# Kernel optimization log

Measured on AMD Instinct MI355X. Metric: run time of the kernel, lower is better.

The kernel has to match this reference:

```python
import jax, jax.numpy as jnp
from jax import lax
import numpy as np

B, T, D, H, W = 1, 32, 32, 64, 64
NE, EXPAND = 4, 2          # num_experts, ffn expand
F = 2 * D                   # real-ified channel count
FH = EXPAND * F
NOISE_SCALE = 0.01
LN_EPS = 1e-5


def _pscan(A, X):
    # first-order linear recurrence y_t = A_t*y_{t-1} + X_t, scan over axis=1
    def comb(l, r):
        a1, x1 = l
        a2, x2 = r
        return (a1 * a2, a2 * x1 + x2)
    return lax.associative_scan(comb, (A, X), axis=1)[1]


def _ln(v, g, b):
    # v: (N, C, H, W); LayerNorm over channel dim (matches permute->LN->permute)
    v = jnp.moveaxis(v, 1, -1)
    m = v.mean(-1, keepdims=True)
    s = v.var(-1, keepdims=True)
    v = (v - m) * lax.rsqrt(s + LN_EPS) * g + b
    return jnp.moveaxis(v, -1, 1)


def setup_inputs() -> dict:
    key = jax.random.key(0)
    ks = jax.random.split(key, 24)
    def rn(i, shape, s=1.0):
        return jax.random.normal(ks[i], shape, jnp.float32) * s
    return {
        "x_re": rn(0, (B, T, D, H, W)),
        "x_im": rn(1, (B, T, D, H, W)),
        "dt": jax.random.uniform(ks[2], (T,), jnp.float32, 0.5, 1.5),
        "eps_re": rn(3, (B, T, H, W, D)),
        "eps_im": rn(4, (B, T, H, W, D)),
        "ln1_g": jnp.ones((F,), jnp.float32), "ln1_b": jnp.zeros((F,), jnp.float32),
        "ln2_g": jnp.ones((F,), jnp.float32), "ln2_b": jnp.zeros((F,), jnp.float32),
        "conv_w": rn(5, (F, F, 3, 3), 0.05), "conv_b": rn(6, (F,), 0.01),
        "enc_re": rn(7, (D, D), D ** -0.5), "enc_im": rn(8, (D, D), D ** -0.5),
        "dec_re": rn(9, (D, D), D ** -0.5), "dec_im": rn(10, (D, D), D ** -0.5),
        "lam_re": rn(11, (D,), 0.5), "lam_im": rn(12, (D,)),
        "flux_alpha": rn(13, (D,)),
        "flux_wre": rn(14, (D, D), 0.1), "flux_wim": rn(15, (D, D), 0.1),
        "wg": rn(16, (F, NE), 0.1),
        "w1": rn(17, (NE, F, FH), 0.05), "b1": jnp.zeros((NE, FH), jnp.float32),
        "w2": rn(18, (NE, FH, F), 0.05), "b2": jnp.zeros((NE, F), jnp.float32),
    }


def reference(x_re, x_im, dt, eps_re, eps_im, ln1_g, ln1_b, ln2_g, ln2_b,
              conv_w, conv_b, enc_re, enc_im, dec_re, dec_im, lam_re, lam_im,
              flux_alpha, flux_wre, flux_wim, wg, w1, b1, w2, b2):
    x = x_re + 1j * x_im                                   # (B,T,D,H,W) complex
    b_, t_, d_, h_, w_ = x.shape
    # --- spatial branch: LN over 2D real channels + Clifford-style conv ---
    xr = jnp.concatenate([x_re, x_im], axis=2).reshape(b_ * t_, 2 * d_, h_, w_)
    xn = _ln(xr, ln1_g, ln1_b)
    xs = lax.conv_general_dilated(xn, conv_w, (1, 1), 'SAME',
                                  dimension_numbers=('NCHW', 'OIHW', 'NCHW'))
    xs = xs + conv_b[None, :, None, None]
    xs_c = xs[:, :d_] + 1j * xs[:, d_:]
    xs5 = xs_c.reshape(b_, t_, d_, h_, w_)
    # --- eigenbasis encode (channels-last complex matmul) ---
    xcl = jnp.transpose(xs5, (0, 1, 3, 4, 2))              # (B,T,H,W,D)
    u = xcl @ (enc_re + 1j * enc_im)
    # --- global flux tracker pscan over T ---
    x_mean = xs5.mean(axis=(-2, -1))                       # (B,T,D) complex
    flux_A = jnp.broadcast_to(jax.nn.sigmoid(flux_alpha).astype(x.dtype), x_mean.shape)
    flux_X = x_mean @ (flux_wre + 1j * flux_wim)
    flux_seq = _pscan(flux_A, flux_X)                      # (B,T,D)
    # --- temporal transition operators per step ---
    lam = -jax.nn.softplus(lam_re) + 1j * lam_im           # (D,) stable decay
    dtc = dt.astype(jnp.float32)[:, None]                  # (T,1)
    op_decay = jnp.exp(lam[None, :] * dtc)                 # (T,D) complex
    op_forcing = (op_decay - 1.0) / lam[None, :]
    u_scaled = u * op_forcing[None, :, None, None, :]
    A_time = jnp.broadcast_to(op_decay[None, :, None, None, :], u.shape)
    Y = _pscan(A_time, u_scaled)                           # (B,T,H,W,D)
    # --- state-dependent stochastic term ---
    eps = eps_re + 1j * eps_im
    noise = NOISE_SCALE * jnp.sqrt(dt)[None, :, None, None, None] * Y * eps
    u_out = Y + noise
    # --- decode + temporal LN ---
    x_out = u_out @ (dec_re + 1j * dec_im)                 # (B,T,H,W,D)
    x_out = jnp.transpose(x_out, (0, 1, 4, 2, 3)).reshape(b_ * t_, d_, h_, w_)
    xo_r = jnp.concatenate([x_out.real, x_out.imag], axis=1)
    xo_n = _ln(xo_r, ln2_g, ln2_b)
    xoc = xo_n[:, :d_] + 1j * xo_n[:, d_:]
    # --- gated dense-MoE FFN on real-ified channels-last features ---
    f = jnp.moveaxis(xo_n, 1, -1)                          # (BT,H,W,2D)
    gate = jax.nn.softmax(f @ wg, axis=-1)                 # (BT,H,W,E)
    hdn = jax.nn.gelu(jnp.einsum('nhwc,ecf->nhwef', f, w1) + b1)
    eo = jnp.einsum('nhwef,efc->nhwec', hdn, w2) + b2
    delta_f = jnp.einsum('nhwec,nhwe->nhwc', eo, gate)
    delta = delta_f[..., :d_] + 1j * delta_f[..., d_:]
    delta = jnp.moveaxis(delta, -1, 1)                     # (BT,D,H,W)
    out = x + (xoc + delta).reshape(b_, t_, d_, h_, w_)
    flux_last = flux_seq[:, -1]
    return (jnp.stack([out.real, out.imag], axis=0),
            jnp.stack([flux_last.real, flux_last.imag], axis=0))
```

## Files before the change

### kernel.cpp

```cpp
#include <hip/hip_runtime.h>
#include <math.h>

#define PX 4096
#define TT 32
#define DD 32
#define CC 64
#define PW 66
#define PPX 4356

typedef __attribute__((ext_vector_type(8))) short short8v;
typedef __attribute__((ext_vector_type(4))) float f32x4;

__device__ __forceinline__ float gelu_fast(float x) {
    float u = x * x;
    float a = x * (1.5957691216057308f + 0.07135481627f * u);
    return x / (1.0f + __expf(-a));
}

__device__ __forceinline__ unsigned short f2b(float x) {
    union { float f; unsigned u; } v; v.f = x;
    unsigned r = v.u + 0x7FFF + ((v.u >> 16) & 1);
    return (unsigned short)(r >> 16);
}

__device__ __forceinline__ float b2f(unsigned short b) {
    union { unsigned u; float f; } v; v.u = ((unsigned)b) << 16;
    return v.f;
}

__global__ __launch_bounds__(256) void k1_ln1(
        const float* __restrict__ xre, const float* __restrict__ xim,
        const float* __restrict__ g, const float* __restrict__ b,
        unsigned short* __restrict__ xpad) {
    int gid = blockIdx.x * 256 + threadIdx.x;
    int t = gid >> 12, px = gid & 4095;
    int row = px >> 6, col = px & 63;
    const float* pr = xre + (size_t)t * DD * PX + px;
    const float* pi = xim + (size_t)t * DD * PX + px;
    float s = 0.f, ss = 0.f;
    #pragma unroll
    for (int d = 0; d < DD; ++d) {
        float vr = pr[d * PX], vi = pi[d * PX];
        s += vr + vi; ss += vr * vr + vi * vi;
    }
    float m = s * (1.f / 64.f);
    float var = ss * (1.f / 64.f) - m * m;
    float rs = rsqrtf(var + 1e-5f);
    unsigned short* o = xpad + ((size_t)t * PPX + (row + 1) * PW + (col + 1)) * 64;
    #pragma unroll
    for (int j = 0; j < 8; ++j) {
        short8v v8;
        #pragma unroll
        for (int dd = 0; dd < 8; ++dd) {
            int ch = j * 8 + dd;
            float v = (ch < 32) ? (pr[ch * PX] - m) * rs * g[ch] + b[ch]
                                : (pi[(ch - 32) * PX] - m) * rs * g[ch] + b[ch];
            v8[dd] = (short)f2b(v);
        }
        *(short8v*)&o[j * 8] = v8;
    }
}

__global__ __launch_bounds__(256) void k0_prep(
        const float* __restrict__ w1, const float* __restrict__ w2,
        const float* __restrict__ convw,
        const float* __restrict__ encre, const float* __restrict__ encim,
        const float* __restrict__ decre, const float* __restrict__ decim,
        unsigned short* __restrict__ w1t, unsigned short* __restrict__ w2t,
        unsigned short* __restrict__ w9t,
        unsigned short* __restrict__ benct, unsigned short* __restrict__ bdect,
        unsigned short* __restrict__ xpad) {
    int gid = blockIdx.x * 256 + threadIdx.x;
    if (gid < 32768) {
        int idx = gid;
        int e = idx >> 13, r = idx & 8191;
        int f = r >> 6, p = r & 63;
        int c = (p & 7) + 8 * ((p >> 3) ^ (f & 7));
        w1t[idx] = f2b(w1[((size_t)e * 64 + c) * 128 + f]);
    } else if (gid < 65536) {
        int idx = gid - 32768;
        int e = idx >> 13, r = idx & 8191;
        int n = r >> 7, p = r & 127;
        int f = (p & 7) + 8 * ((p >> 3) ^ (n & 7));
        w2t[idx] = f2b(w2[((size_t)e * 128 + f) * 64 + n]);
    } else if (gid < 102400) {
        int idx = gid - 65536;
        int tap = idx >> 12, rem = idx & 4095;
        int n = rem >> 6, p = rem & 63;
        int k = (p & 7) + 8 * ((p >> 3) ^ (n & 7));
        w9t[idx] = f2b(convw[((size_t)n * 64 + k) * 9 + tap]);
    } else if (gid < 110592) {
        int idx = gid - 102400;
        const float* Rr = (idx < 4096) ? encre : decre;
        const float* Ri = (idx < 4096) ? encim : decim;
        unsigned short* dst = (idx < 4096) ? benct : bdect;
        idx &= 4095;
        int n = idx >> 6, p = idx & 63;
        int k = (p & 7) + 8 * ((p >> 3) ^ (n & 7));
        float v;
        if (n < 32) v = (k < 32) ? Rr[k * 32 + n] : -Ri[(k - 32) * 32 + n];
        else        v = (k < 32) ? Ri[k * 32 + (n - 32)] : Rr[(k - 32) * 32 + (n - 32)];
        dst[idx] = f2b(v);
    } else if (gid < 110592 + 32 * 260) {
        int idx = gid - 110592;
        int im = idx / 260, h = idx % 260;
        int row, col;
        if (h < 66)       { row = 0;  col = h; }
        else if (h < 132) { row = 65; col = h - 66; }
        else { int hh = h - 132; row = 1 + (hh >> 1); col = (hh & 1) * 65; }
        unsigned short* p = xpad + ((size_t)im * PPX + row * PW + col) * 64;
        short8v z = (short8v)0;
        #pragma unroll
        for (int j = 0; j < 8; ++j) *(short8v*)&p[j * 8] = z;
    }
}

__global__ __launch_bounds__(256, 2) void k2_conv(
        const unsigned short* __restrict__ xpad,
        const unsigned short* __restrict__ w9t,
        const float* __restrict__ bias, float* __restrict__ xs) {
    __shared__ __align__(16) unsigned short wst[36864];
    int tid = threadIdx.x;
    int bid = blockIdx.x;
    int lb = (bid & 7) * 64 + (bid >> 3);
    int t = lb >> 4, rg = lb & 15;
    int lane = tid & 63, wv = tid >> 6;
    int l15 = lane & 15, g = lane >> 4;
    #pragma unroll
    for (int i = 0; i < 18; ++i) {
        int idx = i * 256 + tid;
        *(short8v*)&wst[idx * 8] = *(const short8v*)&w9t[idx * 8];
    }
    __syncthreads();
    int r = rg * 4 + wv;
    const unsigned short* xb = xpad + (size_t)t * PPX * 64;
    f32x4 acc[4][4];
    #pragma unroll
    for (int m = 0; m < 4; ++m)
        #pragma unroll
        for (int nt = 0; nt < 4; ++nt) acc[m][nt] = (f32x4)0.f;

    #pragma unroll
    for (int kh = 0; kh < 3; ++kh) {
        #pragma unroll
        for (int kw = 0; kw < 3; ++kw) {
            int tap = kh * 3 + kw;
            #pragma unroll
            for (int kc = 0; kc < 2; ++kc) {
                short8v a[4];
                #pragma unroll
                for (int m = 0; m < 4; ++m) {
                    int pcol = m * 16 + l15 + kw;
                    a[m] = *(const short8v*)&xb[((size_t)(r + kh) * PW + pcol) * 64 + kc * 32 + g * 8];
                }
                #pragma unroll
                for (int nt = 0; nt < 4; ++nt) {
                    int n = nt * 16 + l15;
                    short8v bf = *(const short8v*)&wst[tap * 4096 + n * 64 + ((kc * 4 + g) ^ (n & 7)) * 8];
                    #pragma unroll
                    for (int m = 0; m < 4; ++m)
                        acc[m][nt] = __builtin_amdgcn_mfma_f32_16x16x32_bf16(a[m], bf, acc[m][nt], 0, 0, 0);
                }
            }
        }
    }
    float* dst = xs + ((size_t)t * PX + r * 64) * 64;
    #pragma unroll
    for (int nt = 0; nt < 4; ++nt) {
        float bo = bias[nt * 16 + l15];
        #pragma unroll
        for (int m = 0; m < 4; ++m) {
            #pragma unroll
            for (int reg = 0; reg < 4; ++reg) {
                int tok = m * 16 + g * 4 + reg;
                dst[(size_t)tok * 64 + nt * 16 + l15] = acc[m][nt][reg] + bo;
            }
        }
    }
}

__global__ __launch_bounds__(256) void k3_mean(
        const float* __restrict__ xs, float* __restrict__ mpart) {
    __shared__ f32x4 red[256];
    int t = blockIdx.x >> 4, sl = blockIdx.x & 15;
    int c4 = threadIdx.x & 15, q = threadIdx.x >> 4;
    const float* base = xs + ((size_t)t * PX + sl * 256) * 64 + c4 * 4;
    f32x4 s = (f32x4)0.f;
    for (int px = q; px < 256; px += 16)
        s += *(const f32x4*)&base[(size_t)px * 64];
    red[threadIdx.x] = s;
    __syncthreads();
    for (int st = 8; st > 0; st >>= 1) {
        if (q < st) red[q * 16 + c4] += red[(q + st) * 16 + c4];
        __syncthreads();
    }
    if (q == 0)
        *(f32x4*)&mpart[((size_t)t * 16 + sl) * 64 + c4 * 4] = red[c4];
}

__global__ __launch_bounds__(256) void k4_ops(
        const float* __restrict__ dt, const float* __restrict__ lam_re,
        const float* __restrict__ lam_im, const float* __restrict__ alpha,
        const float* __restrict__ wre, const float* __restrict__ wim,
        const float* __restrict__ mpart, float* __restrict__ tabs,
        float* __restrict__ outflux) {
    __shared__ float meanl[2048];
    int tid = threadIdx.x;
    for (int idx = tid; idx < 2048; idx += 256) {
        int t = idx >> 6, c = idx & 63;
        float s = 0.f;
        #pragma unroll
        for (int p = 0; p < 16; ++p) s += mpart[((size_t)t * 16 + p) * 64 + c];
        meanl[idx] = s * (1.f / 4096.f);
    }
    __syncthreads();
    for (int idx = tid; idx < 1024; idx += 256) {
        int t = idx >> 5, d = idx & 31;
        float x = lam_re[d];
        float sp = (x > 0.f) ? x + log1pf(expf(-x)) : log1pf(expf(x));
        float lr = -sp, li = lam_im[d];
        float dtv = dt[t];
        float er = expf(lr * dtv);
        float dr = er * cosf(li * dtv);
        float di = er * sinf(li * dtv);
        float den = lr * lr + li * li;
        float fr = ((dr - 1.f) * lr + di * li) / den;
        float fi = (di * lr - (dr - 1.f) * li) / den;
        tabs[idx] = dr; tabs[1024 + idx] = di;
        tabs[2048 + idx] = fr; tabs[3072 + idx] = fi;
    }
    if (tid < 32) {
        int d = tid;
        float a = 1.f / (1.f + expf(-alpha[d]));
        float yr = 0.f, yi = 0.f;
        for (int t = 0; t < 32; ++t) {
            float xr = 0.f, xi = 0.f;
            for (int k = 0; k < 32; ++k) {
                float mr = meanl[t * 64 + k], mi = meanl[t * 64 + 32 + k];
                float wr = wre[k * 32 + d], wi = wim[k * 32 + d];
                xr += mr * wr - mi * wi;
                xi += mr * wi + mi * wr;
            }
            yr = a * yr + xr; yi = a * yi + xi;
        }
        outflux[d] = yr; outflux[32 + d] = yi;
    }
}

template<bool FORCING>
__global__ __launch_bounds__(256) void k5_gemm(
        const float* A, const unsigned short* __restrict__ Bt,
        const float* __restrict__ tabs, float* O) {
    __shared__ __align__(16) unsigned short fA[64 * 64];
    __shared__ __align__(16) unsigned short bst[64 * 64];
    int tid = threadIdx.x;
    int lane = tid & 63, wv = tid >> 6;
    int l15 = lane & 15, g = lane >> 4;
    int row0 = wv * 16 + l15;
    int rowb = wv * 16 + g * 4;
    #pragma unroll
    for (int i = 0; i < 2; ++i)
        *(short8v*)&bst[(i * 256 + tid) * 8] = *(const short8v*)&Bt[(i * 256 + tid) * 8];

    #pragma unroll
    for (int tile = 0; tile < 2; ++tile) {
        size_t tok0 = ((size_t)blockIdx.x * 2 + tile) * 64;
        if (tile) __syncthreads();
        #pragma unroll
        for (int r = 0; r < 16; ++r) {
            int idx = r * 256 + tid;
            int tok = idx >> 6, c = idx & 63;
            fA[tok * 64 + (c & 7) + 8 * ((c >> 3) ^ (tok & 7))] = f2b(A[(tok0 + tok) * 64 + c]);
        }
        __syncthreads();
        short8v a1[2];
        #pragma unroll
        for (int st = 0; st < 2; ++st)
            a1[st] = *(const short8v*)&fA[row0 * 64 + (((st * 4 + g) ^ (row0 & 7))) * 8];
        f32x4 eo[4];
        #pragma unroll
        for (int i = 0; i < 4; ++i) eo[i] = (f32x4)0.f;
        #pragma unroll
        for (int st = 0; st < 2; ++st) {
            #pragma unroll
            for (int nt = 0; nt < 4; ++nt) {
                int n = nt * 16 + l15;
                short8v b = *(const short8v*)&bst[n * 64 + (((st * 4 + g) ^ (n & 7))) * 8];
                eo[nt] = __builtin_amdgcn_mfma_f32_16x16x32_bf16(a1[st], b, eo[nt], 0, 0, 0);
            }
        }
        if (FORCING) {
            int t = (int)(tok0 >> 12);
            #pragma unroll
            for (int p = 0; p < 2; ++p) {
                int d = p * 16 + l15;
                float fr = tabs[2048 + t * 32 + d], fi = tabs[3072 + t * 32 + d];
                #pragma unroll
                for (int r = 0; r < 4; ++r) {
                    float ur = eo[p][r], ui = eo[p + 2][r];
                    eo[p][r]     = ur * fr - ui * fi;
                    eo[p + 2][r] = ur * fi + ui * fr;
                }
            }
        }
        #pragma unroll
        for (int nt = 0; nt < 4; ++nt) {
            int n = nt * 16 + l15;
            #pragma unroll
            for (int r = 0; r < 4; ++r)
                O[(tok0 + rowb + r) * 64 + n] = eo[nt][r];
        }
    }
}

__global__ __launch_bounds__(256) void k5b_scan(
        float* U, const float* __restrict__ tabs, const float* __restrict__ dt,
        const float* __restrict__ eps_re, const float* __restrict__ eps_im) {
    int gid = blockIdx.x * 256 + threadIdx.x;
    int px = gid >> 5, d = gid & 31;
    float Yr = 0.f, Yi = 0.f;
    for (int t = 0; t < TT; ++t) {
        size_t tok = (size_t)t * PX + px;
        float usr = U[tok * 64 + d], usi = U[tok * 64 + 32 + d];
        float dr = tabs[t * 32 + d], di = tabs[1024 + t * 32 + d];
        float nYr = dr * Yr - di * Yi + usr;
        float nYi = dr * Yi + di * Yr + usi;
        Yr = nYr; Yi = nYi;
        float s = 0.01f * sqrtf(dt[t]);
        size_t ei = tok * 32 + d;
        float epr = eps_re[ei], epi = eps_im[ei];
        U[tok * 64 + d]      = Yr + s * (Yr * epr - Yi * epi);
        U[tok * 64 + 32 + d] = Yi + s * (Yr * epi + Yi * epr);
    }
}

__global__ __launch_bounds__(256, 4) void k6_moe(
        const float* __restrict__ xo,
        const float* __restrict__ g2, const float* __restrict__ b2ln,
        const float* __restrict__ wg,
        const unsigned short* __restrict__ w1t, const float* __restrict__ b1,
        const unsigned short* __restrict__ w2t, const float* __restrict__ b2m,
        const float* __restrict__ xre, const float* __restrict__ xim,
        float* __restrict__ out) {
    __shared__ __align__(16) float hdl[64 * 65];
    __shared__ __align__(16) unsigned short wst[8192];
    __shared__ float wgl[256];
    unsigned short* H = (unsigned short*)hdl;

    int tid = threadIdx.x;
    int lane = tid & 63;
    int wv = tid >> 6;
    int l15 = lane & 15, g = lane >> 4;
    int t = blockIdx.x >> 6;
    int px0 = (blockIdx.x & 63) * 64;
    int tok = wv * 16 + l15;
    int tsw = tok & 7;

    wgl[tid] = wg[tid];

    float f[16];
    {
        const float* src = xo + ((size_t)t * PX + px0 + tok) * 64 + g * 8;
        #pragma unroll
        for (int st = 0; st < 2; ++st) {
            float4 v0 = *(const float4*)&src[st * 32];
            float4 v1 = *(const float4*)&src[st * 32 + 4];
            f[st*8+0]=v0.x; f[st*8+1]=v0.y; f[st*8+2]=v0.z; f[st*8+3]=v0.w;
            f[st*8+4]=v1.x; f[st*8+5]=v1.y; f[st*8+6]=v1.z; f[st*8+7]=v1.w;
        }
    }
    float s = 0.f, ss = 0.f;
    #pragma unroll
    for (int i = 0; i < 16; ++i) { s += f[i]; ss += f[i] * f[i]; }
    s += __shfl_xor(s, 16); ss += __shfl_xor(ss, 16);
    s += __shfl_xor(s, 32); ss += __shfl_xor(ss, 32);
    float m = s * (1.f / 64.f);
    float rs = rsqrtf(ss * (1.f / 64.f) - m * m + 1e-5f);
    #pragma unroll
    for (int st = 0; st < 2; ++st) {
        int c0 = st * 32 + g * 8;
        float4 gv0 = *(const float4*)&g2[c0],   gv1 = *(const float4*)&g2[c0 + 4];
        float4 bv0 = *(const float4*)&b2ln[c0], bv1 = *(const float4*)&b2ln[c0 + 4];
        f[st*8+0] = (f[st*8+0]-m)*rs*gv0.x + bv0.x;
        f[st*8+1] = (f[st*8+1]-m)*rs*gv0.y + bv0.y;
        f[st*8+2] = (f[st*8+2]-m)*rs*gv0.z + bv0.z;
        f[st*8+3] = (f[st*8+3]-m)*rs*gv0.w + bv0.w;
        f[st*8+4] = (f[st*8+4]-m)*rs*gv1.x + bv1.x;
        f[st*8+5] = (f[st*8+5]-m)*rs*gv1.y + bv1.y;
        f[st*8+6] = (f[st*8+6]-m)*rs*gv1.z + bv1.z;
        f[st*8+7] = (f[st*8+7]-m)*rs*gv1.w + bv1.w;
    }
    __syncthreads();
    float gt[4];
    {
        float g0 = 0.f, g1 = 0.f, g2_ = 0.f, g3 = 0.f;
        #pragma unroll
        for (int st = 0; st < 2; ++st)
            #pragma unroll
            for (int j = 0; j < 8; ++j) {
                int c = st * 32 + g * 8 + j;
                float fv = f[st * 8 + j];
                g0 += fv * wgl[c*4];   g1 += fv * wgl[c*4+1];
                g2_ += fv * wgl[c*4+2]; g3 += fv * wgl[c*4+3];
            }
        g0 += __shfl_xor(g0, 16); g1 += __shfl_xor(g1, 16);
        g2_ += __shfl_xor(g2_, 16); g3 += __shfl_xor(g3, 16);
        g0 += __shfl_xor(g0, 32); g1 += __shfl_xor(g1, 32);
        g2_ += __shfl_xor(g2_, 32); g3 += __shfl_xor(g3, 32);
        float mx = fmaxf(fmaxf(g0, g1), fmaxf(g2_, g3));
        float e0 = expf(g0-mx), e1 = expf(g1-mx), e2 = expf(g2_-mx), e3 = expf(g3-mx);
        float inv = 1.f / (e0 + e1 + e2 + e3);
        gt[0] = e0*inv; gt[1] = e1*inv; gt[2] = e2*inv; gt[3] = e3*inv;
    }
    short8v bf1[2];
    #pragma unroll
    for (int st = 0; st < 2; ++st)
        #pragma unroll
        for (int j = 0; j < 8; ++j)
            bf1[st][j] = (short)f2b(f[st * 8 + j]);

    f32x4 dacc[4];
    #pragma unroll
    for (int i = 0; i < 4; ++i) dacc[i] = (f32x4)0.f;

    for (int e = 0; e < 4; ++e) {
        __syncthreads();
        {
            const short8v* gp = (const short8v*)(w1t + (size_t)e * 8192);
            #pragma unroll
            for (int i = 0; i < 4; ++i)
                *(short8v*)&wst[(i * 256 + tid) * 8] = gp[i * 256 + tid];
        }
        __syncthreads();
        f32x4 h[8];
        #pragma unroll
        for (int i = 0; i < 8; ++i) h[i] = (f32x4)0.f;
        #pragma unroll
        for (int st = 0; st < 2; ++st) {
            #pragma unroll
            for (int ft = 0; ft < 8; ++ft) {
                int fi = ft * 16 + l15;
                short8v a = *(const short8v*)&wst[fi * 64 + (((st * 4 + g) ^ (fi & 7))) * 8];
                h[ft] = __builtin_amdgcn_mfma_f32_16x16x32_bf16(a, bf1[st], h[ft], 0, 0, 0);
            }
        }
        #pragma unroll
        for (int ft = 0; ft < 8; ++ft) {
            int f0 = ft * 16 + g * 4;
            float4 bb = *(const float4*)&b1[e * 128 + f0];
            unsigned short p0 = f2b(gelu_fast(h[ft][0] + bb.x));
            unsigned short p1 = f2b(gelu_fast(h[ft][1] + bb.y));
            unsigned short p2 = f2b(gelu_fast(h[ft][2] + bb.z));
            unsigned short p3 = f2b(gelu_fast(h[ft][3] + bb.w));
            unsigned long long pk = (unsigned long long)p0 | ((unsigned long long)p1 << 16)
                                  | ((unsigned long long)p2 << 32) | ((unsigned long long)p3 << 48);
            *(unsigned long long*)&H[tok * 128 + (f0 & 7) + 8 * ((f0 >> 3) ^ tsw)] = pk;
        }
        __syncthreads();
        {
            const short8v* gp = (const short8v*)(w2t + (size_t)e * 8192);
            #pragma unroll
            for (int i = 0; i < 4; ++i)
                *(short8v*)&wst[(i * 256 + tid) * 8] = gp[i * 256 + tid];
        }
        __syncthreads();
        f32x4 eo[4];
        #pragma unroll
        for (int i = 0; i < 4; ++i) eo[i] = (f32x4)0.f;
        #pragma unroll
        for (int st = 0; st < 4; ++st) {
            short8v bh = *(const short8v*)&H[tok * 128 + (((st * 4 + g) ^ tsw)) * 8];
            #pragma unroll
            for (int nt = 0; nt < 4; ++nt) {
                int n = nt * 16 + l15;
                short8v a = *(const short8v*)&wst[n * 128 + (((st * 4 + g) ^ (n & 7))) * 8];
                eo[nt] = __builtin_amdgcn_mfma_f32_16x16x32_bf16(a, bh, eo[nt], 0, 0, 0);
            }
        }
        float ge = gt[e];
        #pragma unroll
        for (int nt = 0; nt < 4; ++nt) {
            int n0 = nt * 16 + g * 4;
            float4 bb = *(const float4*)&b2m[e * 64 + n0];
            dacc[nt][0] += ge * (eo[nt][0] + bb.x);
            dacc[nt][1] += ge * (eo[nt][1] + bb.y);
            dacc[nt][2] += ge * (eo[nt][2] + bb.z);
            dacc[nt][3] += ge * (eo[nt][3] + bb.w);
        }
    }
    __syncthreads();
    float* dl = hdl;
    #pragma unroll
    for (int nt = 0; nt < 4; ++nt) {
        int n0 = nt * 16 + g * 4;
        #pragma unroll
        for (int r = 0; r < 4; ++r)
            dl[tok * 65 + n0 + r] = dacc[nt][r];
    }
    __syncthreads();
    #pragma unroll
    for (int st = 0; st < 2; ++st) {
        const float* xsrc = (st == 0) ? xre : xim;
        float* osrc = out + (st == 0 ? 0 : (size_t)4194304);
        #pragma unroll
        for (int j = 0; j < 8; ++j) {
            int c = st * 32 + g * 8 + j;
            float val = b2f((unsigned short)bf1[st][j]) + dl[tok * 65 + c];
            size_t xi_ = ((size_t)t * 32 + (c & 31)) * PX + px0 + tok;
            osrc[xi_] = val + xsrc[xi_];
        }
    }
}

extern "C" void kernel_launch(void* const* d_in, const int* in_sizes, int n_in,
                              void* d_out, int out_size, void* d_ws, size_t ws_size,
                              hipStream_t stream) {
    const float* xre   = (const float*)d_in[0];
    const float* xim   = (const float*)d_in[1];
    const float* dt    = (const float*)d_in[2];
    const float* epsre = (const float*)d_in[3];
    const float* epsim = (const float*)d_in[4];
    const float* ln1g  = (const float*)d_in[5];
    const float* ln1b  = (const float*)d_in[6];
    const float* ln2g  = (const float*)d_in[7];
    const float* ln2b  = (const float*)d_in[8];
    const float* convw = (const float*)d_in[9];
    const float* convb = (const float*)d_in[10];
    const float* encre = (const float*)d_in[11];
    const float* encim = (const float*)d_in[12];
    const float* decre = (const float*)d_in[13];
    const float* decim = (const float*)d_in[14];
    const float* lamre = (const float*)d_in[15];
    const float* lamim = (const float*)d_in[16];
    const float* alpha = (const float*)d_in[17];
    const float* fwre  = (const float*)d_in[18];
    const float* fwim  = (const float*)d_in[19];
    const float* wg    = (const float*)d_in[20];
    const float* w1    = (const float*)d_in[21];
    const float* b1    = (const float*)d_in[22];
    const float* w2    = (const float*)d_in[23];
    const float* b2    = (const float*)d_in[24];
    float* out = (float*)d_out;

    float* ws = (float*)d_ws;
    unsigned short* xpad = (unsigned short*)ws;
    float* xo   = ws;
    float* xs   = ws + 8388608;
    float* tabs = ws + 16779264;
    unsigned short* w1t = (unsigned short*)(ws + 16783360);
    unsigned short* w2t = w1t + 32768;
    unsigned short* w9t = w2t + 32768;
    unsigned short* benct = w9t + 36864;
    unsigned short* bdect = benct + 4096;
    float* mpart = ws + 16783360 + 55296;

    k0_prep<<<465, 256, 0, stream>>>(w1, w2, convw, encre, encim, decre, decim,
                                     w1t, w2t, w9t, benct, bdect, xpad);
    k1_ln1<<<512, 256, 0, stream>>>(xre, xim, ln1g, ln1b, xpad);
    k2_conv<<<512, 256, 0, stream>>>(xpad, w9t, convb, xs);
    k3_mean<<<512, 256, 0, stream>>>(xs, mpart);
    k4_ops<<<1, 256, 0, stream>>>(dt, lamre, lamim, alpha, fwre, fwim, mpart,
                                  tabs, out + 8388608);
    k5_gemm<true><<<1024, 256, 0, stream>>>(xs, benct, tabs, xs);
    k5b_scan<<<512, 256, 0, stream>>>(xs, tabs, dt, epsre, epsim);
    k5_gemm<false><<<1024, 256, 0, stream>>>(xs, bdect, tabs, xo);
    k6_moe<<<2048, 256, 0, stream>>>(xo, ln2g, ln2b, wg, w1t, b1, w2t, b2,
                                     xre, xim, out);
}
```

Before: 197.5 us.

## Fuse channel-mean reduction into encode GEMM and move decay tables to prep

Removes the separate mean-reduction kernel by accumulating per-channel partial sums while the encode GEMM loads its input tile, writing 32 partials per timestep to mpart. The decay and forcing table computation moves into the prep kernel, so the single-block flux kernel only computes the flux and runs after the decode GEMM. This drops one full read of the conv output and one serialized single-block launch from the critical path. The cost is a small block reduction added to the GEMM.

```diff
diff --git a/kernel.cpp b/kernel.cpp
--- a/kernel.cpp
+++ b/kernel.cpp
@@ -66,10 +66,12 @@
         const float* __restrict__ convw,
         const float* __restrict__ encre, const float* __restrict__ encim,
         const float* __restrict__ decre, const float* __restrict__ decim,
+        const float* __restrict__ dt, const float* __restrict__ lam_re,
+        const float* __restrict__ lam_im,
         unsigned short* __restrict__ w1t, unsigned short* __restrict__ w2t,
         unsigned short* __restrict__ w9t,
         unsigned short* __restrict__ benct, unsigned short* __restrict__ bdect,
-        unsigned short* __restrict__ xpad) {
+        unsigned short* __restrict__ xpad, float* __restrict__ tabs) {
     int gid = blockIdx.x * 256 + threadIdx.x;
     if (gid < 32768) {
         int idx = gid;
@@ -101,7 +103,7 @@
         if (n < 32) v = (k < 32) ? Rr[k * 32 + n] : -Ri[(k - 32) * 32 + n];
         else        v = (k < 32) ? Ri[k * 32 + (n - 32)] : Rr[(k - 32) * 32 + (n - 32)];
         dst[idx] = f2b(v);
-    } else if (gid < 110592 + 32 * 260) {
+    } else if (gid < 118912) {
         int idx = gid - 110592;
         int im = idx / 260, h = idx % 260;
         int row, col;
@@ -112,6 +114,21 @@
         short8v z = (short8v)0;
         #pragma unroll
         for (int j = 0; j < 8; ++j) *(short8v*)&p[j * 8] = z;
+    } else if (gid < 119936) {
+        int idx = gid - 118912;
+        int t = idx >> 5, d = idx & 31;
+        float x = lam_re[d];
+        float sp = (x > 0.f) ? x + log1pf(expf(-x)) : log1pf(expf(x));
+        float lr = -sp, li = lam_im[d];
+        float dtv = dt[t];
+        float er = expf(lr * dtv);
+        float dr = er * cosf(li * dtv);
+        float di = er * sinf(li * dtv);
+        float den = lr * lr + li * li;
+        float fr = ((dr - 1.f) * lr + di * li) / den;
+        float fi = (di * lr - (dr - 1.f) * li) / den;
+        tabs[idx] = dr; tabs[1024 + idx] = di;
+        tabs[2048 + idx] = fr; tabs[3072 + idx] = fi;
     }
 }
 
@@ -179,56 +196,20 @@
     }
 }
 
-__global__ __launch_bounds__(256) void k3_mean(
-        const float* __restrict__ xs, float* __restrict__ mpart) {
-    __shared__ f32x4 red[256];
-    int t = blockIdx.x >> 4, sl = blockIdx.x & 15;
-    int c4 = threadIdx.x & 15, q = threadIdx.x >> 4;
-    const float* base = xs + ((size_t)t * PX + sl * 256) * 64 + c4 * 4;
-    f32x4 s = (f32x4)0.f;
-    for (int px = q; px < 256; px += 16)
-        s += *(const f32x4*)&base[(size_t)px * 64];
-    red[threadIdx.x] = s;
-    __syncthreads();
-    for (int st = 8; st > 0; st >>= 1) {
-        if (q < st) red[q * 16 + c4] += red[(q + st) * 16 + c4];
-        __syncthreads();
-    }
-    if (q == 0)
-        *(f32x4*)&mpart[((size_t)t * 16 + sl) * 64 + c4 * 4] = red[c4];
-}
-
-__global__ __launch_bounds__(256) void k4_ops(
-        const float* __restrict__ dt, const float* __restrict__ lam_re,
-        const float* __restrict__ lam_im, const float* __restrict__ alpha,
+__global__ __launch_bounds__(256) void k4_flux(
+        const float* __restrict__ alpha,
         const float* __restrict__ wre, const float* __restrict__ wim,
-        const float* __restrict__ mpart, float* __restrict__ tabs,
-        float* __restrict__ outflux) {
+        const float* __restrict__ mpart, float* __restrict__ outflux) {
     __shared__ float meanl[2048];
     int tid = threadIdx.x;
     for (int idx = tid; idx < 2048; idx += 256) {
         int t = idx >> 6, c = idx & 63;
         float s = 0.f;
         #pragma unroll
-        for (int p = 0; p < 16; ++p) s += mpart[((size_t)t * 16 + p) * 64 + c];
+        for (int p = 0; p < 32; ++p) s += mpart[((size_t)t * 32 + p) * 64 + c];
         meanl[idx] = s * (1.f / 4096.f);
     }
     __syncthreads();
-    for (int idx = tid; idx < 1024; idx += 256) {
-        int t = idx >> 5, d = idx & 31;
-        float x = lam_re[d];
-        float sp = (x > 0.f) ? x + log1pf(expf(-x)) : log1pf(expf(x));
-        float lr = -sp, li = lam_im[d];
-        float dtv = dt[t];
-        float er = expf(lr * dtv);
-        float dr = er * cosf(li * dtv);
-        float di = er * sinf(li * dtv);
-        float den = lr * lr + li * li;
-        float fr = ((dr - 1.f) * lr + di * li) / den;
-        float fi = (di * lr - (dr - 1.f) * li) / den;
-        tabs[idx] = dr; tabs[1024 + idx] = di;
-        tabs[2048 + idx] = fr; tabs[3072 + idx] = fi;
-    }
     if (tid < 32) {
         int d = tid;
         float a = 1.f / (1.f + expf(-alpha[d]));
@@ -250,9 +231,10 @@
 template<bool FORCING>
 __global__ __launch_bounds__(256) void k5_gemm(
         const float* A, const unsigned short* __restrict__ Bt,
-        const float* __restrict__ tabs, float* O) {
+        const float* __restrict__ tabs, float* O, float* __restrict__ mpart) {
     __shared__ __align__(16) unsigned short fA[64 * 64];
     __shared__ __align__(16) unsigned short bst[64 * 64];
+    __shared__ float red[256];
     int tid = threadIdx.x;
     int lane = tid & 63, wv = tid >> 6;
     int l15 = lane & 15, g = lane >> 4;
@@ -262,6 +244,7 @@
     for (int i = 0; i < 2; ++i)
         *(short8v*)&bst[(i * 256 + tid) * 8] = *(const short8v*)&Bt[(i * 256 + tid) * 8];
 
+    float msum = 0.f;
     #pragma unroll
     for (int tile = 0; tile < 2; ++tile) {
         size_t tok0 = ((size_t)blockIdx.x * 2 + tile) * 64;
@@ -270,7 +253,9 @@
         for (int r = 0; r < 16; ++r) {
             int idx = r * 256 + tid;
             int tok = idx >> 6, c = idx & 63;
-            fA[tok * 64 + (c & 7) + 8 * ((c >> 3) ^ (tok & 7))] = f2b(A[(tok0 + tok) * 64 + c]);
+            float v = A[(tok0 + tok) * 64 + c];
+            if (FORCING) msum += v;
+            fA[tok * 64 + (c & 7) + 8 * ((c >> 3) ^ (tok & 7))] = f2b(v);
         }
         __syncthreads();
         short8v a1[2];
@@ -310,6 +295,14 @@
             for (int r = 0; r < 4; ++r)
                 O[(tok0 + rowb + r) * 64 + n] = eo[nt][r];
         }
+    }
+    if (FORCING) {
+        __syncthreads();
+        red[tid] = msum;
+        __syncthreads();
+        if (tid < 64)
+            mpart[(size_t)blockIdx.x * 64 + tid] =
+                red[tid] + red[tid + 64] + red[tid + 128] + red[tid + 192];
     }
 }
 
@@ -554,16 +547,15 @@
     unsigned short* bdect = benct + 4096;
     float* mpart = ws + 16783360 + 55296;
 
-    k0_prep<<<465, 256, 0, stream>>>(w1, w2, convw, encre, encim, decre, decim,
-                                     w1t, w2t, w9t, benct, bdect, xpad);
+    k0_prep<<<469, 256, 0, stream>>>(w1, w2, convw, encre, encim, decre, decim,
+                                     dt, lamre, lamim,
+                                     w1t, w2t, w9t, benct, bdect, xpad, tabs);
     k1_ln1<<<512, 256, 0, stream>>>(xre, xim, ln1g, ln1b, xpad);
     k2_conv<<<512, 256, 0, stream>>>(xpad, w9t, convb, xs);
-    k3_mean<<<512, 256, 0, stream>>>(xs, mpart);
-    k4_ops<<<1, 256, 0, stream>>>(dt, lamre, lamim, alpha, fwre, fwim, mpart,
-                                  tabs, out + 8388608);
-    k5_gemm<true><<<1024, 256, 0, stream>>>(xs, benct, tabs, xs);
+    k5_gemm<true><<<1024, 256, 0, stream>>>(xs, benct, tabs, xs, mpart);
     k5b_scan<<<512, 256, 0, stream>>>(xs, tabs, dt, epsre, epsim);
-    k5_gemm<false><<<1024, 256, 0, stream>>>(xs, bdect, tabs, xo);
+    k5_gemm<false><<<1024, 256, 0, stream>>>(xs, bdect, tabs, xo, nullptr);
+    k4_flux<<<1, 256, 0, stream>>>(alpha, fwre, fwim, mpart, out + 8388608);
     k6_moe<<<2048, 256, 0, stream>>>(xo, ln2g, ln2b, wg, w1t, b1, w2t, b2,
                                      xre, xim, out);
 }
```

Result: faster. 189.8 us (-3.9%).
